# Kernel optimization log

Hardware: AMD Instinct MI355X
Metric: run time of the kernel (lower is better)

The kernel has to match this reference:

```python
import jax, jax.numpy as jnp
import numpy as np

ROPE_BASE = 10000.0

def _rms_norm(x):
    eps = jnp.asarray(jnp.finfo(x.dtype).eps, x.dtype)
    return x * jax.lax.rsqrt(jnp.mean(x * x, axis=-1, keepdims=True) + eps)

def _rope(x):
    # x: [B, S, H, hd]; rotate-halves variant: y1 = x1*cos + x2*sin, y2 = -x1*sin + x2*cos
    S, hd = x.shape[1], x.shape[3]
    d = hd // 2
    inv_freq = 1.0 / (ROPE_BASE ** (jnp.arange(0, hd, 2, dtype=jnp.float32) / hd))  # [d]
    t = jnp.arange(S, dtype=jnp.float32)
    freqs = jnp.outer(t, inv_freq)                       # [S, d]
    cos = jnp.cos(freqs)[None, :, None, :].astype(x.dtype)
    sin = jnp.sin(freqs)[None, :, None, :].astype(x.dtype)
    x1, x2 = x[..., :d], x[..., d:]
    return jnp.concatenate([x1 * cos + x2 * sin, -x1 * sin + x2 * cos], axis=-1)

def setup_inputs() -> dict:
    key = jax.random.key(0)
    ks = jax.random.split(key, 7)
    B, S, D = 1, 2048, 1024
    std = 0.02
    return {
        "x": jax.random.normal(ks[0], (B, S, D), jnp.float32),
        "v1": jax.random.normal(ks[1], (B, S, D), jnp.float32),
        "Wq": jax.random.normal(ks[2], (D, D), jnp.float32) * std,
        "Wk": jax.random.normal(ks[3], (D, D), jnp.float32) * std,
        "Wv": jax.random.normal(ks[4], (D, D), jnp.float32) * std,
        "Wout": jax.random.normal(ks[5], (D, D), jnp.float32) * std,
        "lambdas": jnp.float32(0.5),
        "n_heads": 16,
    }

def reference(x, v1, Wq, Wk, Wv, Wout, lambdas, n_heads):
    B, S, D = x.shape
    H = n_heads
    hd = D // H
    # QKV projections (CastedLinear, no bias)
    q = (x @ Wq.T).reshape(B, S, H, hd)
    k = (x @ Wk.T).reshape(B, S, H, hd)
    v = (x @ Wv.T).reshape(B, S, H, hd)
    # value residual mix with first-layer values v1
    v = (1.0 - lambdas) * v + lambdas * v1.reshape(B, S, H, hd)
    # per-head RMS norm (no learned scale) then RoPE
    q, k = _rms_norm(q), _rms_norm(k)
    q, k = _rope(q), _rope(k)
    # causal attention (flex_attention default: softmax, scale 1/sqrt(hd))
    scale = 1.0 / jnp.sqrt(jnp.asarray(hd, x.dtype))
    scores = jnp.einsum('bqhd,bkhd->bhqk', q, k) * scale        # [B,H,S,S]
    causal = jnp.tril(jnp.ones((S, S), dtype=bool))
    scores = jnp.where(causal[None, None], scores, jnp.asarray(-jnp.inf, scores.dtype))
    p = jax.nn.softmax(scores, axis=-1)
    y = jnp.einsum('bhqk,bkhd->bqhd', p, v).reshape(B, S, D)
    y = y @ Wout.T
    return (y, v1)
```

## Files before the change

kernel.cpp:

```cpp
#include <hip/hip_runtime.h>
#include <hip/hip_bf16.h>

#define S_LEN 2048
#define D_DIM 1024
#define NH    16
#define NEG_BIG (-1.0e30f)

#define EPI_NORMROPE   1
#define EPI_VMIX_T     2
#define EPI_F32        3
#define EPI_NORMROPE_Q 4
#define EPI_F32A       5

typedef __attribute__((ext_vector_type(8))) short bf16x8;
typedef __attribute__((ext_vector_type(4))) float f32x4;
typedef const __attribute__((address_space(1))) unsigned char gu8_t;
typedef __attribute__((address_space(3))) unsigned char lu8_t;

__device__ __forceinline__ float bf2f(unsigned short h) {
    union { unsigned int u; float f; } v; v.u = ((unsigned int)h) << 16; return v.f;
}
__device__ __forceinline__ unsigned short f2b(float f) {
    union { float f; unsigned int u; } v; v.f = f;
    unsigned int u = v.u;
    return (unsigned short)((u + 0x7FFFu + ((u >> 16) & 1u)) >> 16);
}
__device__ __forceinline__ unsigned short f2b_trunc(float f) {
    union { float f; unsigned int u; } v; v.f = f;
    return (unsigned short)(v.u >> 16);
}

__global__ __launch_bounds__(256)
void to_bf16(const float* __restrict__ x,  const float* __restrict__ wq,
             const float* __restrict__ wk, const float* __restrict__ wv,
             const float* __restrict__ wo,
             unsigned short* __restrict__ xb,  unsigned short* __restrict__ wqb,
             unsigned short* __restrict__ wkb, unsigned short* __restrict__ wvb,
             unsigned short* __restrict__ wob)
{
    const int z = blockIdx.y;
    const float* s; unsigned short* d; int n;
    switch (z) {
        case 0: s = x;  d = xb;  n = S_LEN * D_DIM; break;
        case 1: s = wq; d = wqb; n = D_DIM * D_DIM; break;
        case 2: s = wk; d = wkb; n = D_DIM * D_DIM; break;
        case 3: s = wv; d = wvb; n = D_DIM * D_DIM; break;
        default: s = wo; d = wob; n = D_DIM * D_DIM; break;
    }
    int i8 = blockIdx.x * 256 + threadIdx.x;
    if (i8 * 8 >= n) return;
    const float* sp = s + (size_t)i8 * 8;
    float4 lo = *(const float4*)sp, hi = *(const float4*)(sp + 4);
    uint4 p;
    p.x = f2b(lo.x) | ((unsigned)f2b(lo.y) << 16);
    p.y = f2b(lo.z) | ((unsigned)f2b(lo.w) << 16);
    p.z = f2b(hi.x) | ((unsigned)f2b(hi.y) << 16);
    p.w = f2b(hi.z) | ((unsigned)f2b(hi.w) << 16);
    *(uint4*)(d + (size_t)i8 * 8) = p;
}

__global__ __launch_bounds__(256, 3)
void gemm64(const unsigned short* __restrict__ A,
            const unsigned short* __restrict__ B0, const unsigned short* __restrict__ B1,
            const unsigned short* __restrict__ B2,
            void* __restrict__ C0, void* __restrict__ C1, void* __restrict__ C2,
            const float* __restrict__ vmix, const float* __restrict__ lam,
            int epiPack)
{
    const int which = blockIdx.z;
    const unsigned short* Bp = (which == 0) ? B0 : ((which == 1) ? B1 : B2);
    void* C = (which == 0) ? C0 : ((which == 1) ? C1 : C2);
    const int epi = (epiPack >> (8 * which)) & 0xff;
    const int tn = blockIdx.x * 128;
    const int tm = blockIdx.y * 64;

    __shared__ unsigned short Asl[64 * 32];
    __shared__ unsigned short Bsl[128 * 32];

    const int t    = threadIdx.x;
    const int lane = t & 63;
    const int wave = t >> 6;
    const int wm   = (wave >> 1) * 32;
    const int wn   = (wave & 1) * 64;
    const int lrow = lane & 15;
    const int quad = lane >> 4;
    const int srow = t >> 2;
    const int scol = (t & 3) * 8;

    f32x4 acc[2][4];
    #pragma unroll
    for (int i = 0; i < 2; ++i)
        #pragma unroll
        for (int j = 0; j < 4; ++j) {
            f32x4 z = {0.f, 0.f, 0.f, 0.f};
            acc[i][j] = z;
        }

    for (int k0 = 0; k0 < D_DIM; k0 += 32) {
        __builtin_amdgcn_global_load_lds(
            (gu8_t*)(A + (size_t)(tm + srow) * D_DIM + k0 + scol),
            (lu8_t*)&Asl[t * 8], 16, 0, 0);
        __builtin_amdgcn_global_load_lds(
            (gu8_t*)(Bp + (size_t)(tn + srow) * D_DIM + k0 + scol),
            (lu8_t*)&Bsl[t * 8], 16, 0, 0);
        __builtin_amdgcn_global_load_lds(
            (gu8_t*)(Bp + (size_t)(tn + 64 + srow) * D_DIM + k0 + scol),
            (lu8_t*)&Bsl[2048 + t * 8], 16, 0, 0);
        __syncthreads();
        bf16x8 af[2], bfr[4];
        #pragma unroll
        for (int i = 0; i < 2; ++i)
            af[i] = *(const bf16x8*)(&Asl[(wm + i * 16 + lrow) * 32 + quad * 8]);
        #pragma unroll
        for (int j = 0; j < 4; ++j)
            bfr[j] = *(const bf16x8*)(&Bsl[(wn + j * 16 + lrow) * 32 + quad * 8]);
        #pragma unroll
        for (int i = 0; i < 2; ++i)
            #pragma unroll
            for (int j = 0; j < 4; ++j)
                acc[i][j] = __builtin_amdgcn_mfma_f32_16x16x32_bf16(af[i], bfr[j], acc[i][j], 0, 0, 0);
        __syncthreads();
    }

    if (epi == EPI_NORMROPE || epi == EPI_NORMROPE_Q) {
        const float post = (epi == EPI_NORMROPE_Q) ? 0.18033688011112042f : 1.0f;
        #pragma unroll
        for (int i = 0; i < 2; ++i) {
            #pragma unroll
            for (int r = 0; r < 4; ++r) {
                int row = tm + wm + i * 16 + quad * 4 + r;
                float v0 = acc[i][0][r], v1 = acc[i][1][r];
                float v2 = acc[i][2][r], v3 = acc[i][3][r];
                float ss = v0 * v0 + v1 * v1 + v2 * v2 + v3 * v3;
                ss += __shfl_xor(ss, 1); ss += __shfl_xor(ss, 2);
                ss += __shfl_xor(ss, 4); ss += __shfl_xor(ss, 8);
                float rms = rsqrtf(ss * (1.f / 64.f) + 1.1920929e-7f) * post;
                v0 *= rms; v1 *= rms; v2 *= rms; v3 *= rms;
                float fs = (float)row;
                float a0 = fs * exp2f(-0.41524101186092030f * (float)lrow);
                float a1 = fs * exp2f(-0.41524101186092030f * (float)(16 + lrow));
                float s0, c0, s1, c1;
                __sincosf(a0, &s0, &c0);
                __sincosf(a1, &s1, &c1);
                unsigned short* Cb = (unsigned short*)C;
                size_t base = (size_t)row * D_DIM + tn + wn + lrow;
                Cb[base]      = f2b(v0 * c0 + v2 * s0);
                Cb[base + 16] = f2b(v1 * c1 + v3 * s1);
                Cb[base + 32] = f2b(-v0 * s0 + v2 * c0);
                Cb[base + 48] = f2b(-v1 * s1 + v3 * c1);
            }
        }
    } else if (epi == EPI_VMIX_T) {
        float lamf = *lam;
        #pragma unroll
        for (int i = 0; i < 2; ++i) {
            int cm0 = tm + wm + i * 16 + quad * 4;
            #pragma unroll
            for (int j = 0; j < 4; ++j) {
                int cn = tn + wn + j * 16 + lrow;
                ushort4 pk;
                float vals[4];
                #pragma unroll
                for (int r = 0; r < 4; ++r) {
                    size_t idx = (size_t)(cm0 + r) * D_DIM + cn;
                    vals[r] = (1.f - lamf) * acc[i][j][r] + lamf * vmix[idx];
                }
                pk.x = f2b(vals[0]); pk.y = f2b(vals[1]);
                pk.z = f2b(vals[2]); pk.w = f2b(vals[3]);
                *(ushort4*)((unsigned short*)C + (size_t)cn * S_LEN + cm0) = pk;
            }
        }
    } else {
        #pragma unroll
        for (int i = 0; i < 2; ++i) {
            int cm0 = tm + wm + i * 16 + quad * 4;
            #pragma unroll
            for (int j = 0; j < 4; ++j) {
                int cn = tn + wn + j * 16 + lrow;
                #pragma unroll
                for (int r = 0; r < 4; ++r)
                    ((float*)C)[(size_t)(cm0 + r) * D_DIM + cn] = acc[i][j][r];
            }
        }
    }
}

__global__ __launch_bounds__(256, 3)
void gemm_bt(const unsigned short* __restrict__ A,
             const unsigned short* __restrict__ B0,
             void* __restrict__ C0,
             const float* __restrict__ lam,
             int epi, int splitK)
{
    const int which = blockIdx.z;
    const unsigned short* Bp = B0;
    void* C = C0;
    int kLo = 0, kHi = D_DIM;
    if (splitK) { kLo = which * (D_DIM / 2); kHi = kLo + D_DIM / 2; }
    const int tn = blockIdx.x * 128;
    const int tm = blockIdx.y * 128;

    __shared__ unsigned short Asl[128 * 32];
    __shared__ unsigned short Bsl[128 * 32];

    const int t    = threadIdx.x;
    const int lane = t & 63;
    const int wave = t >> 6;
    const int wm   = (wave >> 1) * 64;
    const int wn   = (wave & 1) * 64;
    const int lrow = lane & 15;
    const int quad = lane >> 4;
    const int srow = lane >> 2;
    const int scol = (lane & 3) * 8;

    f32x4 acc[4][4];
    #pragma unroll
    for (int i = 0; i < 4; ++i)
        #pragma unroll
        for (int j = 0; j < 4; ++j) {
            f32x4 z = {0.f, 0.f, 0.f, 0.f};
            acc[i][j] = z;
        }

    for (int k0 = kLo; k0 < kHi; k0 += 32) {
        #pragma unroll
        for (int rep = 0; rep < 2; ++rep) {
            int grp = wave * 2 + rep;
            int row = grp * 16 + srow;
            __builtin_amdgcn_global_load_lds(
                (gu8_t*)(A + (size_t)(tm + row) * D_DIM + k0 + scol),
                (lu8_t*)&Asl[grp * 512], 16, 0, 0);
            __builtin_amdgcn_global_load_lds(
                (gu8_t*)(Bp + (size_t)(tn + row) * D_DIM + k0 + scol),
                (lu8_t*)&Bsl[grp * 512], 16, 0, 0);
        }
        __syncthreads();
        bf16x8 af[4], bfr[4];
        #pragma unroll
        for (int i = 0; i < 4; ++i)
            af[i] = *(const bf16x8*)(&Asl[(wm + i * 16 + lrow) * 32 + quad * 8]);
        #pragma unroll
        for (int j = 0; j < 4; ++j)
            bfr[j] = *(const bf16x8*)(&Bsl[(wn + j * 16 + lrow) * 32 + quad * 8]);
        #pragma unroll
        for (int i = 0; i < 4; ++i)
            #pragma unroll
            for (int j = 0; j < 4; ++j)
                acc[i][j] = __builtin_amdgcn_mfma_f32_16x16x32_bf16(af[i], bfr[j], acc[i][j], 0, 0, 0);
        __syncthreads();
    }

    if (epi == EPI_F32A) {
        #pragma unroll
        for (int i = 0; i < 4; ++i) {
            int cm0 = tm + wm + i * 16 + quad * 4;
            #pragma unroll
            for (int j = 0; j < 4; ++j) {
                int cn = tn + wn + j * 16 + lrow;
                #pragma unroll
                for (int r = 0; r < 4; ++r)
                    atomicAdd(&((float*)C)[(size_t)(cm0 + r) * D_DIM + cn], acc[i][j][r]);
            }
        }
    } else {
        #pragma unroll
        for (int i = 0; i < 4; ++i) {
            int cm0 = tm + wm + i * 16 + quad * 4;
            #pragma unroll
            for (int j = 0; j < 4; ++j) {
                int cn = tn + wn + j * 16 + lrow;
                #pragma unroll
                for (int r = 0; r < 4; ++r)
                    ((float*)C)[(size_t)(cm0 + r) * D_DIM + cn] = acc[i][j][r];
            }
        }
    }
}

__global__ __launch_bounds__(256, 3)
void attn_mfma(const unsigned short* Qb,
               const unsigned short* __restrict__ Kb,
               const unsigned short* __restrict__ Vtg,
               float* __restrict__ Opart, float* __restrict__ Lpart)
{
    const int bx = blockIdx.x;
    int qt, c;
    if (bx < 32)      { qt = 31 - (bx >> 2);            c = bx & 3;  }
    else if (bx < 56) { int i = bx - 32; qt = 23 - i/3; c = i % 3;   }
    else if (bx < 72) { int i = bx - 56; qt = 15 - (i>>1); c = i & 1;}
    else              { qt = 7 - (bx - 72);             c = 0;       }
    const int jlo = c * 8;
    const int jhi = min(jlo + 7, qt);
    const int h  = blockIdx.y;
    const int t  = threadIdx.x;
    const int w  = t >> 6;
    const int l  = t & 63;
    const int l15  = l & 15;
    const int quad = l >> 4;
    const int hco  = h * 64;
    const int slot = (qt * 4 + c) * NH + h;

    __shared__ unsigned short Ks[2][64][72];
    __shared__ unsigned short Vt[2][64][72];
    __shared__ unsigned short Ps[4][16][72];

    const unsigned short* qrow = Qb + (size_t)(qt * 64 + w * 16 + l15) * D_DIM + hco;
    bf16x8 qf0 = *(const bf16x8*)(qrow + quad * 8);
    bf16x8 qf1 = *(const bf16x8*)(qrow + 32 + quad * 8);

    f32x4 oac[4];
    #pragma unroll
    for (int nt = 0; nt < 4; ++nt) { f32x4 z = {0.f,0.f,0.f,0.f}; oac[nt] = z; }
    float lsum = 0.f;

    const int rr = t >> 2;
    const int dc = (t & 3) * 16;

    const unsigned short* kbase = Kb  + (size_t)rr * D_DIM + hco + dc;
    const unsigned short* vbase = Vtg + (size_t)(hco + rr) * S_LEN + dc;

    uint4 ka0, ka1, va0, va1;
    {
        const unsigned short* kp = kbase + (size_t)jlo * 64 * D_DIM;
        const unsigned short* vp = vbase + (size_t)jlo * 64;
        ka0 = *(const uint4*)kp;  ka1 = *(const uint4*)(kp + 8);
        va0 = *(const uint4*)vp;  va1 = *(const uint4*)(vp + 8);
    }

    const int q_g = qt * 64 + w * 16 + l15;
    const float C2 = -11.541560327111707f;

    for (int j = jlo; j <= jhi; ++j) {
        const int buf = (j - jlo) & 1;
        *(uint4*)&Ks[buf][rr][dc]     = ka0;
        *(uint4*)&Ks[buf][rr][dc + 8] = ka1;
        *(uint4*)&Vt[buf][rr][dc]     = va0;
        *(uint4*)&Vt[buf][rr][dc + 8] = va1;
        __syncthreads();
        if (j < jhi) {
            const unsigned short* kp = kbase + (size_t)(j + 1) * 64 * D_DIM;
            const unsigned short* vp = vbase + (size_t)(j + 1) * 64;
            ka0 = *(const uint4*)kp;  ka1 = *(const uint4*)(kp + 8);
            va0 = *(const uint4*)vp;  va1 = *(const uint4*)(vp + 8);
        }

        f32x4 sac[4];
        __builtin_amdgcn_s_setprio(1);
        #pragma unroll
        for (int nt = 0; nt < 4; ++nt) {
            f32x4 z = {0.f,0.f,0.f,0.f};
            bf16x8 kf0 = *(const bf16x8*)&Ks[buf][nt * 16 + l15][quad * 8];
            z = __builtin_amdgcn_mfma_f32_16x16x32_bf16(kf0, qf0, z, 0, 0, 0);
            bf16x8 kf1 = *(const bf16x8*)&Ks[buf][nt * 16 + l15][32 + quad * 8];
            z = __builtin_amdgcn_mfma_f32_16x16x32_bf16(kf1, qf1, z, 0, 0, 0);
            sac[nt] = z;
        }
        __builtin_amdgcn_s_setprio(0);

        if (j < qt) {
            #pragma unroll
            for (int nt = 0; nt < 4; ++nt) {
                float pe0 = exp2f(sac[nt][0] + C2);
                float pe1 = exp2f(sac[nt][1] + C2);
                float pe2 = exp2f(sac[nt][2] + C2);
                float pe3 = exp2f(sac[nt][3] + C2);
                lsum += (pe0 + pe1) + (pe2 + pe3);
                ushort4 pk;
                pk.x = f2b_trunc(pe0); pk.y = f2b_trunc(pe1);
                pk.z = f2b_trunc(pe2); pk.w = f2b_trunc(pe3);
                *(ushort4*)&Ps[w][l15][nt * 16 + quad * 4] = pk;
            }
        } else {
            #pragma unroll
            for (int nt = 0; nt < 4; ++nt) {
                int key0 = j * 64 + nt * 16 + quad * 4;
                float pe[4];
                #pragma unroll
                for (int r = 0; r < 4; ++r) {
                    float s = sac[nt][r] + C2;
                    if (key0 + r > q_g) s = NEG_BIG;
                    pe[r] = exp2f(s);
                    lsum += pe[r];
                }
                ushort4 pk;
                pk.x = f2b_trunc(pe[0]); pk.y = f2b_trunc(pe[1]);
                pk.z = f2b_trunc(pe[2]); pk.w = f2b_trunc(pe[3]);
                *(ushort4*)&Ps[w][l15][nt * 16 + quad * 4] = pk;
            }
        }

        bf16x8 pf0 = *(const bf16x8*)&Ps[w][l15][quad * 8];
        bf16x8 pf1 = *(const bf16x8*)&Ps[w][l15][32 + quad * 8];
        __builtin_amdgcn_s_setprio(1);
        #pragma unroll
        for (int nt = 0; nt < 4; ++nt) {
            bf16x8 vf0 = *(const bf16x8*)&Vt[buf][nt * 16 + l15][quad * 8];
            oac[nt] = __builtin_amdgcn_mfma_f32_16x16x32_bf16(pf0, vf0, oac[nt], 0, 0, 0);
            bf16x8 vf1 = *(const bf16x8*)&Vt[buf][nt * 16 + l15][32 + quad * 8];
            oac[nt] = __builtin_amdgcn_mfma_f32_16x16x32_bf16(pf1, vf1, oac[nt], 0, 0, 0);
        }
        __builtin_amdgcn_s_setprio(0);
    }

    float lr = lsum;
    lr += __shfl_xor(lr, 16);
    lr += __shfl_xor(lr, 32);
    if (l < 16)
        Lpart[(size_t)slot * 64 + w * 16 + l15] = lr;
    float* Op = Opart + (size_t)slot * 4096;
    #pragma unroll
    for (int nt = 0; nt < 4; ++nt)
        #pragma unroll
        for (int r = 0; r < 4; ++r)
            Op[(size_t)(w * 16 + quad * 4 + r) * 64 + nt * 16 + l15] = oac[nt][r];
}

__global__ __launch_bounds__(256)
void attn_combine(const float* __restrict__ Opart, const float* __restrict__ Lpart,
                  unsigned short* __restrict__ Ob, float* __restrict__ yzero)
{
    const int qt  = blockIdx.x;
    const int h   = blockIdx.y;
    const int t   = threadIdx.x;
    const int row = t >> 2;
    const int c0  = (t & 3) * 16;
    float acc[16];
    #pragma unroll
    for (int i = 0; i < 16; ++i) acc[i] = 0.f;
    float lsum = 0.f;
    for (int c = 0; c < 4; ++c) {
        if (c * 8 > qt) break;
        const size_t slot = (size_t)((qt * 4 + c) * NH + h);
        const float* Op = Opart + slot * 4096 + (size_t)row * 64 + c0;
        #pragma unroll
        for (int g = 0; g < 4; ++g) {
            float4 a = *(const float4*)(Op + g * 4);
            acc[g * 4 + 0] += a.x; acc[g * 4 + 1] += a.y;
            acc[g * 4 + 2] += a.z; acc[g * 4 + 3] += a.w;
        }
        lsum += Lpart[slot * 64 + row];
    }
    const float inv = 1.f / lsum;
    unsigned int pk[8];
    #pragma unroll
    for (int i = 0; i < 8; ++i)
        pk[i] = f2b(acc[2 * i] * inv) | ((unsigned)f2b(acc[2 * i + 1] * inv) << 16);
    unsigned short* dst = Ob + (size_t)(qt * 64 + row) * D_DIM + h * 64 + c0;
    *(uint4*)dst       = make_uint4(pk[0], pk[1], pk[2], pk[3]);
    *(uint4*)(dst + 8) = make_uint4(pk[4], pk[5], pk[6], pk[7]);

    const int flat = (h * 32 + qt) * 256 + t;
    float4 z4 = {0.f, 0.f, 0.f, 0.f};
    float4* yz = (float4*)(yzero + (size_t)flat * 16);
    yz[0] = z4; yz[1] = z4; yz[2] = z4; yz[3] = z4;
}

__global__ __launch_bounds__(256)
void copy_v1(const uint4* __restrict__ src, uint4* __restrict__ dst) {
    int i = blockIdx.x * 256 + threadIdx.x;
    dst[i] = src[i];
}

extern "C" void kernel_launch(void* const* d_in, const int* in_sizes, int n_in,
                              void* d_out, int out_size, void* d_ws, size_t ws_size,
                              hipStream_t stream)
{
    const float* x    = (const float*)d_in[0];
    const float* v1   = (const float*)d_in[1];
    const float* Wq   = (const float*)d_in[2];
    const float* Wk   = (const float*)d_in[3];
    const float* Wv   = (const float*)d_in[4];
    const float* Wout = (const float*)d_in[5];
    const float* lam  = (const float*)d_in[6];
    float* out = (float*)d_out;

    const size_t SD = (size_t)S_LEN * D_DIM;
    const size_t DD = (size_t)D_DIM * D_DIM;
    unsigned short* Qb  = (unsigned short*)d_ws;
    unsigned short* Kb  = Qb + SD;
    unsigned short* Vtg = Kb + SD;
    unsigned short* Ab  = Qb;
    float* Opart = (float*)(Vtg + SD);
    float* Lpart = Opart + (size_t)2048 * 4096;

    unsigned short* Wqb   = (unsigned short*)d_out;
    unsigned short* Wkb   = Wqb + DD;
    unsigned short* Wvb   = Wkb + DD;
    unsigned short* xb    = (unsigned short*)(out + SD);
    unsigned short* Woutb = xb + SD;

    to_bf16<<<dim3(1024, 5), 256, 0, stream>>>(
        x, Wq, Wk, Wv, Wout, xb, Wqb, Wkb, Wvb, Woutb);

    gemm64<<<dim3(D_DIM / 128, S_LEN / 64, 3), 256, 0, stream>>>(
        xb, Wqb, Wkb, Wvb, Qb, Kb, Vtg, v1, lam,
        EPI_NORMROPE_Q | (EPI_NORMROPE << 8) | (EPI_VMIX_T << 16));

    attn_mfma<<<dim3(80, NH), 256, 0, stream>>>(Qb, Kb, Vtg, Opart, Lpart);
    attn_combine<<<dim3(S_LEN / 64, NH), 256, 0, stream>>>(Opart, Lpart, Ab, out);

    gemm_bt<<<dim3(D_DIM / 128, S_LEN / 128, 2), 256, 0, stream>>>(
        Ab, Woutb, d_out, lam, EPI_F32A, 1);

    copy_v1<<<dim3((unsigned)(SD / 4 / 256)), 256, 0, stream>>>(
        (const uint4*)v1, (uint4*)(out + SD));
}
```

Baseline: 176.0 us.

## Alias P scratch into idle K buffer, raise attention occupancy, fold v1 copy

The attention kernel drops its separate P staging buffer and reuses the idle half of the double-buffered K tile. This shrinks LDS use so the launch bound can ask for 4 blocks per CU instead of 3. To keep that reuse safe it adds a __syncthreads at the end of every key-tile iteration. Separately, the v1 passthrough copy is folded into the bf16 conversion launch as a sixth grid slice, and xb/Woutb move into workspace so the copy can happen early, saving one kernel launch.

```diff
diff --git a/kernel.cpp b/kernel.cpp
--- a/kernel.cpp
+++ b/kernel.cpp
@@ -33,12 +33,20 @@
 __global__ __launch_bounds__(256)
 void to_bf16(const float* __restrict__ x,  const float* __restrict__ wq,
              const float* __restrict__ wk, const float* __restrict__ wv,
-             const float* __restrict__ wo,
+             const float* __restrict__ wo, const float* __restrict__ v1,
              unsigned short* __restrict__ xb,  unsigned short* __restrict__ wqb,
              unsigned short* __restrict__ wkb, unsigned short* __restrict__ wvb,
-             unsigned short* __restrict__ wob)
+             unsigned short* __restrict__ wob, float* __restrict__ v1dst)
 {
     const int z = blockIdx.y;
+    int i8 = blockIdx.x * 256 + threadIdx.x;
+    if (z == 5) {
+        const float* sp = v1 + (size_t)i8 * 8;
+        float4 lo = *(const float4*)sp, hi = *(const float4*)(sp + 4);
+        float* dp = v1dst + (size_t)i8 * 8;
+        *(float4*)dp = lo; *(float4*)(dp + 4) = hi;
+        return;
+    }
     const float* s; unsigned short* d; int n;
     switch (z) {
         case 0: s = x;  d = xb;  n = S_LEN * D_DIM; break;
@@ -47,7 +55,6 @@
         case 3: s = wv; d = wvb; n = D_DIM * D_DIM; break;
         default: s = wo; d = wob; n = D_DIM * D_DIM; break;
     }
-    int i8 = blockIdx.x * 256 + threadIdx.x;
     if (i8 * 8 >= n) return;
     const float* sp = s + (size_t)i8 * 8;
     float4 lo = *(const float4*)sp, hi = *(const float4*)(sp + 4);
@@ -277,7 +284,7 @@
     }
 }
 
-__global__ __launch_bounds__(256, 3)
+__global__ __launch_bounds__(256, 4)
 void attn_mfma(const unsigned short* Qb,
                const unsigned short* __restrict__ Kb,
                const unsigned short* __restrict__ Vtg,
@@ -302,7 +309,6 @@
 
     __shared__ unsigned short Ks[2][64][72];
     __shared__ unsigned short Vt[2][64][72];
-    __shared__ unsigned short Ps[4][16][72];
 
     const unsigned short* qrow = Qb + (size_t)(qt * 64 + w * 16 + l15) * D_DIM + hco;
     bf16x8 qf0 = *(const bf16x8*)(qrow + quad * 8);
@@ -357,6 +363,8 @@
         }
         __builtin_amdgcn_s_setprio(0);
 
+        unsigned short (*Psw)[72] = (unsigned short (*)[72])&Ks[buf ^ 1][w * 16];
+
         if (j < qt) {
             #pragma unroll
             for (int nt = 0; nt < 4; ++nt) {
@@ -368,7 +376,7 @@
                 ushort4 pk;
                 pk.x = f2b_trunc(pe0); pk.y = f2b_trunc(pe1);
                 pk.z = f2b_trunc(pe2); pk.w = f2b_trunc(pe3);
-                *(ushort4*)&Ps[w][l15][nt * 16 + quad * 4] = pk;
+                *(ushort4*)&Psw[l15][nt * 16 + quad * 4] = pk;
             }
         } else {
             #pragma unroll
@@ -385,12 +393,12 @@
                 ushort4 pk;
                 pk.x = f2b_trunc(pe[0]); pk.y = f2b_trunc(pe[1]);
                 pk.z = f2b_trunc(pe[2]); pk.w = f2b_trunc(pe[3]);
-                *(ushort4*)&Ps[w][l15][nt * 16 + quad * 4] = pk;
-            }
-        }
-
-        bf16x8 pf0 = *(const bf16x8*)&Ps[w][l15][quad * 8];
-        bf16x8 pf1 = *(const bf16x8*)&Ps[w][l15][32 + quad * 8];
+                *(ushort4*)&Psw[l15][nt * 16 + quad * 4] = pk;
+            }
+        }
+
+        bf16x8 pf0 = *(const bf16x8*)&Psw[l15][quad * 8];
+        bf16x8 pf1 = *(const bf16x8*)&Psw[l15][32 + quad * 8];
         __builtin_amdgcn_s_setprio(1);
         #pragma unroll
         for (int nt = 0; nt < 4; ++nt) {
@@ -400,6 +408,7 @@
             oac[nt] = __builtin_amdgcn_mfma_f32_16x16x32_bf16(pf1, vf1, oac[nt], 0, 0, 0);
         }
         __builtin_amdgcn_s_setprio(0);
+        __syncthreads();
     }
 
     float lr = lsum;
@@ -455,12 +464,6 @@
     yz[0] = z4; yz[1] = z4; yz[2] = z4; yz[3] = z4;
 }
 
-__global__ __launch_bounds__(256)
-void copy_v1(const uint4* __restrict__ src, uint4* __restrict__ dst) {
-    int i = blockIdx.x * 256 + threadIdx.x;
-    dst[i] = src[i];
-}
-
 extern "C" void kernel_launch(void* const* d_in, const int* in_sizes, int n_in,
                               void* d_out, int out_size, void* d_ws, size_t ws_size,
                               hipStream_t stream)
@@ -482,15 +485,15 @@
     unsigned short* Ab  = Qb;
     float* Opart = (float*)(Vtg + SD);
     float* Lpart = Opart + (size_t)2048 * 4096;
+    unsigned short* xb    = (unsigned short*)((char*)d_ws + (46u << 20));
+    unsigned short* Woutb = (unsigned short*)((char*)d_ws + (50u << 20));
 
     unsigned short* Wqb   = (unsigned short*)d_out;
     unsigned short* Wkb   = Wqb + DD;
     unsigned short* Wvb   = Wkb + DD;
-    unsigned short* xb    = (unsigned short*)(out + SD);
-    unsigned short* Woutb = xb + SD;
-
-    to_bf16<<<dim3(1024, 5), 256, 0, stream>>>(
-        x, Wq, Wk, Wv, Wout, xb, Wqb, Wkb, Wvb, Woutb);
+
+    to_bf16<<<dim3(1024, 6), 256, 0, stream>>>(
+        x, Wq, Wk, Wv, Wout, v1, xb, Wqb, Wkb, Wvb, Woutb, out + SD);
 
     gemm64<<<dim3(D_DIM / 128, S_LEN / 64, 3), 256, 0, stream>>>(
         xb, Wqb, Wkb, Wvb, Qb, Kb, Vtg, v1, lam,
@@ -501,7 +504,4 @@
 
     gemm_bt<<<dim3(D_DIM / 128, S_LEN / 128, 2), 256, 0, stream>>>(
         Ab, Woutb, d_out, lam, EPI_F32A, 1);
-
-    copy_v1<<<dim3((unsigned)(SD / 4 / 256)), 256, 0, stream>>>(
-        (const uint4*)v1, (uint4*)(out + SD));
-}
+}
```

Result: no change. 173.4 us (-1.4%).
